# Optimization experiments

Measured on AMD Instinct MI355X. Metric: run time of the kernel, lower is better.

The kernel has to match this reference:

```python
import jax, jax.numpy as jnp
import numpy as np

BS, SEQ, IN, H, L = 32, 512, 1024, 1024, 2
STDV = 1.0 / np.sqrt(H)


def setup_inputs() -> dict:
    key = jax.random.key(0)
    ks = jax.random.split(key, 5)
    # params are uniform(-stdv, stdv) per reset_parameters
    u = lambda k, shape: jax.random.uniform(k, shape, jnp.float32, -STDV, STDV)
    return {
        "x": jax.random.normal(ks[0], (BS, SEQ, IN), jnp.float32),
        "w_ih": u(ks[1], (L, H, IN)),   # layer 0: [H, IN]; layer >0 uses [H, H] (IN==H here)
        "w_hh": u(ks[2], (L, H, H)),
        "b_ih": u(ks[3], (L, H)),
        "b_hh": u(ks[4], (L, H)),
    }


def _run_layer(x_sbH, w_ih_l, w_hh_l, b_ih_l, b_hh_l):
    # x_sbH: [seq, bs, in]. Precompute input projection as one GEMM.
    xproj = jnp.einsum('sbi,hi->sbh', x_sbH, w_ih_l) + b_ih_l + b_hh_l  # [seq, bs, H]

    def step(h, xp_t):
        # h_t = tanh(W_ih x_t + b_ih + W_hh h_{t-1} + b_hh)
        h_new = jnp.tanh(xp_t + h @ w_hh_l.T)
        return h_new, h_new

    h0 = jnp.zeros((x_sbH.shape[1], w_hh_l.shape[0]), x_sbH.dtype)
    h_last, hs = jax.lax.scan(step, h0, xproj)
    return hs, h_last  # hs: [seq, bs, H]


def reference(x, w_ih, w_hh, b_ih, b_hh):
    # batch_first: transpose to [seq, bs, in]
    h = jnp.transpose(x, (1, 0, 2))
    finals = []
    num_layers = w_ih.shape[0]
    for l in range(num_layers):
        h, h_last = _run_layer(h, w_ih[l], w_hh[l], b_ih[l], b_hh[l])
        finals.append(h_last)
    output = jnp.transpose(h, (1, 0, 2))           # [bs, seq, H]
    h_n = jnp.stack(finals, axis=0)                # [num_layers, bs, H]
    return output, h_n
```

## Files before the change

kernel.cpp:

```cpp
#include <hip/hip_runtime.h>

#define SEQL 512
#define BSZ  32
#define HID  1024
#define NWORK 48
#define NLAUNCH 384
#define HN_OFF 16777216

#define XPS_OFF 0u
#define H0B_OFF 33554432u
#define H1B_OFF 67108864u
#define FLG_OFF 100663296u
#define BOOT_OFF 100794368u

using f32x4  = __attribute__((ext_vector_type(4))) float;
using u16x8  = __attribute__((ext_vector_type(8))) unsigned short;
using u32x4  = __attribute__((ext_vector_type(4))) unsigned int;
using bf16x8 = __attribute__((ext_vector_type(8))) __bf16;

__device__ __forceinline__ f32x4 mfma16(u16x8 a, u16x8 b, f32x4 c) {
  return __builtin_amdgcn_mfma_f32_16x16x32_bf16(
      __builtin_bit_cast(bf16x8, a), __builtin_bit_cast(bf16x8, b), c, 0, 0, 0);
}

__device__ __forceinline__ unsigned short f2bf(float f) {
  unsigned u = __builtin_bit_cast(unsigned, f);
  u += 0x7fffu + ((u >> 16) & 1u);
  return (unsigned short)(u >> 16);
}
__device__ __forceinline__ unsigned short f2h(float f) {
  _Float16 h = (_Float16)f;
  return __builtin_bit_cast(unsigned short, h);
}
__device__ __forceinline__ float h2f(unsigned short u) {
  return (float)__builtin_bit_cast(_Float16, u);
}

__device__ __forceinline__ float tanh_fast(float x) {
  float cx = fminf(fmaxf(x, -15.f), 15.f);
  float e = __expf(2.f * cx);
  return __fdividef(e - 1.f, e + 1.f);
}

__device__ __forceinline__ void ld_tile_sc0(const unsigned short* base, u32x4 (&r)[16]) {
  const char* b0 = (const char*)base;
  const char* b1 = b0 + 16 * HID * 2;
  asm volatile(
    "global_load_dwordx4 %0, %16, off sc0\n\t"
    "global_load_dwordx4 %1, %16, off offset:64 sc0\n\t"
    "global_load_dwordx4 %2, %16, off offset:128 sc0\n\t"
    "global_load_dwordx4 %3, %16, off offset:192 sc0\n\t"
    "global_load_dwordx4 %4, %16, off offset:256 sc0\n\t"
    "global_load_dwordx4 %5, %16, off offset:320 sc0\n\t"
    "global_load_dwordx4 %6, %16, off offset:384 sc0\n\t"
    "global_load_dwordx4 %7, %16, off offset:448 sc0\n\t"
    "global_load_dwordx4 %8, %17, off sc0\n\t"
    "global_load_dwordx4 %9, %17, off offset:64 sc0\n\t"
    "global_load_dwordx4 %10, %17, off offset:128 sc0\n\t"
    "global_load_dwordx4 %11, %17, off offset:192 sc0\n\t"
    "global_load_dwordx4 %12, %17, off offset:256 sc0\n\t"
    "global_load_dwordx4 %13, %17, off offset:320 sc0\n\t"
    "global_load_dwordx4 %14, %17, off offset:384 sc0\n\t"
    "global_load_dwordx4 %15, %17, off offset:448 sc0\n\t"
    "s_waitcnt vmcnt(0)"
    : "=&v"(r[0]), "=&v"(r[1]), "=&v"(r[2]), "=&v"(r[3]),
      "=&v"(r[4]), "=&v"(r[5]), "=&v"(r[6]), "=&v"(r[7]),
      "=&v"(r[8]), "=&v"(r[9]), "=&v"(r[10]), "=&v"(r[11]),
      "=&v"(r[12]), "=&v"(r[13]), "=&v"(r[14]), "=&v"(r[15])
    : "v"(b0), "v"(b1)
    : "memory");
}

__device__ __forceinline__ u16x8 ld8h_sc0(const void* p) {
  u32x4 r;
  asm volatile("global_load_dwordx4 %0, %1, off sc0\n\ts_waitcnt vmcnt(0)"
               : "=&v"(r) : "v"(p) : "memory");
  return __builtin_bit_cast(u16x8, r);
}

__device__ __forceinline__ void flag_set(unsigned* p) {
  __hip_atomic_store(p, 1u, __ATOMIC_RELAXED, __HIP_MEMORY_SCOPE_AGENT);
}
__device__ __forceinline__ unsigned flag_get(const unsigned* p) {
  return __hip_atomic_load(p, __ATOMIC_RELAXED, __HIP_MEMORY_SCOPE_AGENT);
}
__device__ __forceinline__ void wave_wait4(const unsigned* flt, int wave, int lane) {
  const unsigned* p = flt + wave * 4 + (lane & 3);
  while (!__all(flag_get(p) != 0u)) {}
}
__device__ __forceinline__ void wave_wait1(const unsigned* p) {
  while (!__all(flag_get(p) != 0u)) {}
}

__global__ void init_kernel(unsigned* flg, int* boot) {
  int i = blockIdx.x * 256 + threadIdx.x;
  flg[i] = 0u;
  if (blockIdx.x == 0) {
    if (threadIdx.x < 16) boot[threadIdx.x] = 0;
    if (threadIdx.x == 16) boot[16] = -1;
  }
}

__global__ __launch_bounds__(256, 2)
void xproj_gemm(const float* __restrict__ X,
                const float* __restrict__ W,
                const float* __restrict__ bih,
                const float* __restrict__ bhh,
                unsigned short* __restrict__ out)
{
  __shared__ unsigned short sA[128 * 32];
  __shared__ unsigned short sB[128 * 32];
  const int tid  = threadIdx.x;
  const int lane = tid & 63;
  const int wave = tid >> 6;
  const int wm = wave >> 1, wn = wave & 1;
  const int bm = blockIdx.x >> 3;
  const int bn = blockIdx.x & 7;
  const int l15 = lane & 15;
  const int koff = (lane >> 4) * 8;
  const int srow = tid >> 2;
  const int skc  = (tid & 3) * 8;

  f32x4 acc[4][4];
#pragma unroll
  for (int i = 0; i < 4; ++i)
#pragma unroll
    for (int j = 0; j < 4; ++j) acc[i][j] = (f32x4)0.f;

  for (int k0 = 0; k0 < HID; k0 += 32) {
#pragma unroll
    for (int r = 0; r < 2; ++r) {
      int row = r * 64 + srow;
      int Mrow = bm * 128 + row;
      const float* src = X + ((size_t)(Mrow & 31) * SEQL + (Mrow >> 5)) * HID + k0 + skc;
      float4 a = ((const float4*)src)[0];
      float4 b = ((const float4*)src)[1];
      u16x8 av;
      av[0]=f2bf(a.x); av[1]=f2bf(a.y); av[2]=f2bf(a.z); av[3]=f2bf(a.w);
      av[4]=f2bf(b.x); av[5]=f2bf(b.y); av[6]=f2bf(b.z); av[7]=f2bf(b.w);
      *(u16x8*)&sA[row * 32 + skc] = av;

      const float* wsrc = W + (size_t)(bn * 128 + row) * HID + k0 + skc;
      float4 wa = ((const float4*)wsrc)[0];
      float4 wb = ((const float4*)wsrc)[1];
      u16x8 wv;
      wv[0]=f2bf(wa.x); wv[1]=f2bf(wa.y); wv[2]=f2bf(wa.z); wv[3]=f2bf(wa.w);
      wv[4]=f2bf(wb.x); wv[5]=f2bf(wb.y); wv[6]=f2bf(wb.z); wv[7]=f2bf(wb.w);
      *(u16x8*)&sB[row * 32 + skc] = wv;
    }
    __syncthreads();

    u16x8 af[4], bfr[4];
#pragma unroll
    for (int mt = 0; mt < 4; ++mt)
      af[mt] = *(const u16x8*)&sA[(wm * 64 + mt * 16 + l15) * 32 + koff];
#pragma unroll
    for (int nt = 0; nt < 4; ++nt)
      bfr[nt] = *(const u16x8*)&sB[(wn * 64 + nt * 16 + l15) * 32 + koff];
#pragma unroll
    for (int mt = 0; mt < 4; ++mt)
#pragma unroll
      for (int nt = 0; nt < 4; ++nt)
        acc[mt][nt] = mfma16(af[mt], bfr[nt], acc[mt][nt]);
    __syncthreads();
  }

#pragma unroll
  for (int nt = 0; nt < 4; ++nt) {
    int colg = bn * 128 + wn * 64 + nt * 16 + l15;
    float bias = bih[colg] + bhh[colg];
#pragma unroll
    for (int mt = 0; mt < 4; ++mt) {
#pragma unroll
      for (int i = 0; i < 4; ++i) {
        int rowg = bm * 128 + wm * 64 + mt * 16 + (lane >> 4) * 4 + i;
        out[(size_t)rowg * HID + colg] = f2h(acc[mt][nt][i] + bias);
      }
    }
  }
}

__global__ __launch_bounds__(256, 2)
void fused_scan(unsigned short* __restrict__ xps,
                const float* __restrict__ whh0,
                const float* __restrict__ wih1,
                const float* __restrict__ whh1,
                const float* __restrict__ bih1,
                const float* __restrict__ bhh1,
                unsigned short* __restrict__ h0b,
                unsigned short* __restrict__ h1b,
                float* __restrict__ out,
                unsigned* __restrict__ flg,
                int* __restrict__ boot)
{
  const int tid  = threadIdx.x;

  __shared__ int s_role;
  if (tid == 0) {
    unsigned xcc;
    asm volatile("s_getreg_b32 %0, hwreg(HW_REG_XCC_ID)" : "=s"(xcc));
    xcc &= 15u;
    int slot = __hip_atomic_fetch_add(&boot[(int)xcc], 1, __ATOMIC_RELAXED,
                                      __HIP_MEMORY_SCOPE_AGENT);
    if (slot == NWORK - 1) {
      int exp = -1;
      __hip_atomic_compare_exchange_strong(&boot[16], &exp, (int)xcc,
          __ATOMIC_RELAXED, __ATOMIC_RELAXED, __HIP_MEMORY_SCOPE_AGENT);
    }
    int ch;
    while ((ch = __hip_atomic_load(&boot[16], __ATOMIC_RELAXED,
                                   __HIP_MEMORY_SCOPE_AGENT)) < 0)
      __builtin_amdgcn_s_sleep(8);
    s_role = ((int)xcc == ch && slot < NWORK) ? slot : -1;
  }
  __syncthreads();
  const int role = s_role;
  if (role < 0) return;

  const int lane = tid & 63;
  const int wave = tid >> 6;
  const int l15  = lane & 15;
  const int l4   = lane >> 4;
  const int stage = role >> 4;
  const int wg    = role & 15;
  const int col0  = wg * 64;
  const int kbase = wave * 256;
  const int frow  = tid >> 3;
  const int fcb   = (tid & 7) * 8;
  const int laneoff = l15 * HID + kbase + l4 * 8;

  unsigned* flA = flg;
  unsigned* flB = flg + SEQL * 16;
  unsigned* flC = flg + 2 * SEQL * 16;

  __shared__ float red[4][32][68];

  const float* Wsl = (stage == 0) ? whh0 : (stage == 1) ? wih1 : whh1;
  u16x8 Bf[4][8];
#pragma unroll
  for (int nt = 0; nt < 4; ++nt)
#pragma unroll
    for (int ks = 0; ks < 8; ++ks) {
      const float* src = Wsl + (size_t)(col0 + nt * 16 + l15) * HID + kbase + ks * 32 + l4 * 8;
      float4 a = ((const float4*)src)[0];
      float4 b = ((const float4*)src)[1];
      u16x8 v;
      v[0]=f2bf(a.x); v[1]=f2bf(a.y); v[2]=f2bf(a.z); v[3]=f2bf(a.w);
      v[4]=f2bf(b.x); v[5]=f2bf(b.y); v[6]=f2bf(b.z); v[7]=f2bf(b.w);
      Bf[nt][ks] = v;
    }

  if (stage == 0) {
    u16x8 xh = *(const u16x8*)(xps + (size_t)frow * HID + col0 + fcb);
    for (int t = 0; t < SEQL; ++t) {
      f32x4 acc[2][4];
#pragma unroll
      for (int m = 0; m < 2; ++m)
#pragma unroll
        for (int n = 0; n < 4; ++n) acc[m][n] = (f32x4)0.f;
      if (t > 0) {
        wave_wait4(flA + (t - 1) * 16, wave, lane);
        u32x4 r[16];
        ld_tile_sc0(h0b + (size_t)(t - 1) * (BSZ * HID) + laneoff, r);
#pragma unroll
        for (int ks = 0; ks < 8; ++ks)
#pragma unroll
          for (int m = 0; m < 2; ++m)
#pragma unroll
            for (int n = 0; n < 4; ++n)
              acc[m][n] = mfma16(__builtin_bit_cast(u16x8, r[m * 8 + ks]), Bf[n][ks], acc[m][n]);
      }
#pragma unroll
      for (int m = 0; m < 2; ++m)
#pragma unroll
        for (int n = 0; n < 4; ++n)
#pragma unroll
          for (int q = 0; q < 4; ++q)
            red[wave][m * 16 + l4 * 4 + q][n * 16 + l15] = acc[m][n][q];
      __syncthreads();
      float hv[8];
#pragma unroll
      for (int jj = 0; jj < 2; ++jj) {
        float4 r0 = *(const float4*)&red[0][frow][fcb + jj * 4];
        float4 r1 = *(const float4*)&red[1][frow][fcb + jj * 4];
        float4 r2 = *(const float4*)&red[2][frow][fcb + jj * 4];
        float4 r3 = *(const float4*)&red[3][frow][fcb + jj * 4];
        hv[jj*4+0] = r0.x + r1.x + r2.x + r3.x;
        hv[jj*4+1] = r0.y + r1.y + r2.y + r3.y;
        hv[jj*4+2] = r0.z + r1.z + r2.z + r3.z;
        hv[jj*4+3] = r0.w + r1.w + r2.w + r3.w;
      }
#pragma unroll
      for (int j = 0; j < 8; ++j) hv[j] = tanh_fast(hv[j] + h2f((unsigned short)xh[j]));
      u16x8 hb;
#pragma unroll
      for (int j = 0; j < 8; ++j) hb[j] = f2bf(hv[j]);
      *(u16x8*)(h0b + (size_t)t * (BSZ * HID) + (size_t)frow * HID + col0 + fcb) = hb;
      if (t == SEQL - 1) {
        float* o = out + HN_OFF + (size_t)frow * HID + col0 + fcb;
        ((float4*)o)[0] = make_float4(hv[0], hv[1], hv[2], hv[3]);
        ((float4*)o)[1] = make_float4(hv[4], hv[5], hv[6], hv[7]);
      } else {
        xh = *(const u16x8*)(xps + ((size_t)(t + 1) * BSZ + frow) * HID + col0 + fcb);
      }
      asm volatile("s_waitcnt vmcnt(0)" ::: "memory");
      __syncthreads();
      if (tid == 0) flag_set(&flA[t * 16 + wg]);
    }
  } else if (stage == 1) {
    float bia[8];
#pragma unroll
    for (int j = 0; j < 8; ++j)
      bia[j] = bih1[col0 + fcb + j] + bhh1[col0 + fcb + j];
    for (int t = 0; t < SEQL; ++t) {
      wave_wait4(flA + t * 16, wave, lane);
      u32x4 r[16];
      ld_tile_sc0(h0b + (size_t)t * (BSZ * HID) + laneoff, r);
      f32x4 acc[2][4];
#pragma unroll
      for (int m = 0; m < 2; ++m)
#pragma unroll
        for (int n = 0; n < 4; ++n) acc[m][n] = (f32x4)0.f;
#pragma unroll
      for (int ks = 0; ks < 8; ++ks)
#pragma unroll
        for (int m = 0; m < 2; ++m)
#pragma unroll
          for (int n = 0; n < 4; ++n)
            acc[m][n] = mfma16(__builtin_bit_cast(u16x8, r[m * 8 + ks]), Bf[n][ks], acc[m][n]);
#pragma unroll
      for (int m = 0; m < 2; ++m)
#pragma unroll
        for (int n = 0; n < 4; ++n)
#pragma unroll
          for (int q = 0; q < 4; ++q)
            red[wave][m * 16 + l4 * 4 + q][n * 16 + l15] = acc[m][n][q];
      __syncthreads();
      float sv[8];
#pragma unroll
      for (int jj = 0; jj < 2; ++jj) {
        float4 r0 = *(const float4*)&red[0][frow][fcb + jj * 4];
        float4 r1 = *(const float4*)&red[1][frow][fcb + jj * 4];
        float4 r2 = *(const float4*)&red[2][frow][fcb + jj * 4];
        float4 r3 = *(const float4*)&red[3][frow][fcb + jj * 4];
        sv[jj*4+0] = r0.x + r1.x + r2.x + r3.x;
        sv[jj*4+1] = r0.y + r1.y + r2.y + r3.y;
        sv[jj*4+2] = r0.z + r1.z + r2.z + r3.z;
        sv[jj*4+3] = r0.w + r1.w + r2.w + r3.w;
      }
      u16x8 xo;
#pragma unroll
      for (int j = 0; j < 8; ++j) xo[j] = f2h(sv[j] + bia[j]);
      *(u16x8*)(xps + ((size_t)t * BSZ + frow) * HID + col0 + fcb) = xo;
      asm volatile("s_waitcnt vmcnt(0)" ::: "memory");
      __syncthreads();
      if (tid == 0) flag_set(&flB[t * 16 + wg]);
    }
  } else {
    for (int t = 0; t < SEQL; ++t) {
      f32x4 acc[2][4];
#pragma unroll
      for (int m = 0; m < 2; ++m)
#pragma unroll
        for (int n = 0; n < 4; ++n) acc[m][n] = (f32x4)0.f;
      if (t > 0) {
        wave_wait4(flC + (t - 1) * 16, wave, lane);
        u32x4 r[16];
        ld_tile_sc0(h1b + (size_t)(t - 1) * (BSZ * HID) + laneoff, r);
#pragma unroll
        for (int ks = 0; ks < 8; ++ks)
#pragma unroll
          for (int m = 0; m < 2; ++m)
#pragma unroll
            for (int n = 0; n < 4; ++n)
              acc[m][n] = mfma16(__builtin_bit_cast(u16x8, r[m * 8 + ks]), Bf[n][ks], acc[m][n]);
      }
#pragma unroll
      for (int m = 0; m < 2; ++m)
#pragma unroll
        for (int n = 0; n < 4; ++n)
#pragma unroll
          for (int q = 0; q < 4; ++q)
            red[wave][m * 16 + l4 * 4 + q][n * 16 + l15] = acc[m][n][q];
      __syncthreads();
      wave_wait1(&flB[t * 16 + wg]);
      u16x8 xq = ld8h_sc0(xps + ((size_t)t * BSZ + frow) * HID + col0 + fcb);
      float hv[8];
#pragma unroll
      for (int jj = 0; jj < 2; ++jj) {
        float4 r0 = *(const float4*)&red[0][frow][fcb + jj * 4];
        float4 r1 = *(const float4*)&red[1][frow][fcb + jj * 4];
        float4 r2 = *(const float4*)&red[2][frow][fcb + jj * 4];
        float4 r3 = *(const float4*)&red[3][frow][fcb + jj * 4];
        hv[jj*4+0] = r0.x + r1.x + r2.x + r3.x;
        hv[jj*4+1] = r0.y + r1.y + r2.y + r3.y;
        hv[jj*4+2] = r0.z + r1.z + r2.z + r3.z;
        hv[jj*4+3] = r0.w + r1.w + r2.w + r3.w;
      }
#pragma unroll
      for (int j = 0; j < 8; ++j) hv[j] = tanh_fast(hv[j] + h2f((unsigned short)xq[j]));
      u16x8 hb;
#pragma unroll
      for (int j = 0; j < 8; ++j) hb[j] = f2bf(hv[j]);
      *(u16x8*)(h1b + (size_t)t * (BSZ * HID) + (size_t)frow * HID + col0 + fcb) = hb;
      float* op = out + ((size_t)frow * SEQL + t) * HID + col0 + fcb;
      ((float4*)op)[0] = make_float4(hv[0], hv[1], hv[2], hv[3]);
      ((float4*)op)[1] = make_float4(hv[4], hv[5], hv[6], hv[7]);
      if (t == SEQL - 1) {
        float* o = out + HN_OFF + BSZ * HID + (size_t)frow * HID + col0 + fcb;
        ((float4*)o)[0] = make_float4(hv[0], hv[1], hv[2], hv[3]);
        ((float4*)o)[1] = make_float4(hv[4], hv[5], hv[6], hv[7]);
      }
      asm volatile("s_waitcnt vmcnt(0)" ::: "memory");
      __syncthreads();
      if (tid == 0) flag_set(&flC[t * 16 + wg]);
    }
  }
}

extern "C" void kernel_launch(void* const* d_in, const int* in_sizes, int n_in,
                              void* d_out, int out_size, void* d_ws, size_t ws_size,
                              hipStream_t stream) {
  const float* x    = (const float*)d_in[0];
  const float* w_ih = (const float*)d_in[1];
  const float* w_hh = (const float*)d_in[2];
  const float* b_ih = (const float*)d_in[3];
  const float* b_hh = (const float*)d_in[4];
  float* out = (float*)d_out;
  char* ws = (char*)d_ws;

  unsigned short* xps = (unsigned short*)(ws + XPS_OFF);
  unsigned short* h0b = (unsigned short*)(ws + H0B_OFF);
  unsigned short* h1b = (unsigned short*)(ws + H1B_OFF);
  unsigned* flg       = (unsigned*)(ws + FLG_OFF);
  int* boot           = (int*)(ws + BOOT_OFF);

  init_kernel<<<96, 256, 0, stream>>>(flg, boot);
  xproj_gemm<<<1024, 256, 0, stream>>>(x, w_ih, b_ih, b_hh, xps);
  fused_scan<<<NLAUNCH, 256, 0, stream>>>(xps, w_hh,
      w_ih + (size_t)HID * HID, w_hh + (size_t)HID * HID,
      b_ih + HID, b_hh + HID, h0b, h1b, out, flg, boot);
}
```

Before: 3.788 ms.

## Replace flag handshakes with sentinel-polled data and merge layer-1 stages

Drops the per-timestep flag arrays. Consumers now poll the hidden-state buffers themselves, which are prefilled with a 0xAA sentinel pattern, and accept a tile once no 32-bit word still matches the sentinel. Producers write with agent-scope atomic 8-byte stores and no longer wait on vmcnt or set a flag. The layer-1 input projection and recurrence stages are merged into one workgroup that holds both weight slices in registers, so 32 workgroups run instead of 48 and the intermediate xps round-trip is gone. The costs are a 64 MB memset on every call, more register pressure (launch bounds lowered to 1), and a small risk of a false wait if a real bf16 pair happens to equal the sentinel.

```diff
diff --git a/kernel.cpp b/kernel.cpp
--- a/kernel.cpp
+++ b/kernel.cpp
@@ -3,19 +3,21 @@
 #define SEQL 512
 #define BSZ  32
 #define HID  1024
-#define NWORK 48
+#define NWORK 32
 #define NLAUNCH 384
 #define HN_OFF 16777216
 
 #define XPS_OFF 0u
 #define H0B_OFF 33554432u
 #define H1B_OFF 67108864u
-#define FLG_OFF 100663296u
-#define BOOT_OFF 100794368u
+#define BOOT_OFF 100663296u
+
+#define SENT32 0xAAAAAAAAu
 
 using f32x4  = __attribute__((ext_vector_type(4))) float;
 using u16x8  = __attribute__((ext_vector_type(8))) unsigned short;
 using u32x4  = __attribute__((ext_vector_type(4))) unsigned int;
+using u64x2  = __attribute__((ext_vector_type(2))) unsigned long long;
 using bf16x8 = __attribute__((ext_vector_type(8))) __bf16;
 
 __device__ __forceinline__ f32x4 mfma16(u16x8 a, u16x8 b, f32x4 c) {
@@ -42,63 +44,45 @@
   return __fdividef(e - 1.f, e + 1.f);
 }
 
-__device__ __forceinline__ void ld_tile_sc0(const unsigned short* base, u32x4 (&r)[16]) {
-  const char* b0 = (const char*)base;
-  const char* b1 = b0 + 16 * HID * 2;
-  asm volatile(
-    "global_load_dwordx4 %0, %16, off sc0\n\t"
-    "global_load_dwordx4 %1, %16, off offset:64 sc0\n\t"
-    "global_load_dwordx4 %2, %16, off offset:128 sc0\n\t"
-    "global_load_dwordx4 %3, %16, off offset:192 sc0\n\t"
-    "global_load_dwordx4 %4, %16, off offset:256 sc0\n\t"
-    "global_load_dwordx4 %5, %16, off offset:320 sc0\n\t"
-    "global_load_dwordx4 %6, %16, off offset:384 sc0\n\t"
-    "global_load_dwordx4 %7, %16, off offset:448 sc0\n\t"
-    "global_load_dwordx4 %8, %17, off sc0\n\t"
-    "global_load_dwordx4 %9, %17, off offset:64 sc0\n\t"
-    "global_load_dwordx4 %10, %17, off offset:128 sc0\n\t"
-    "global_load_dwordx4 %11, %17, off offset:192 sc0\n\t"
-    "global_load_dwordx4 %12, %17, off offset:256 sc0\n\t"
-    "global_load_dwordx4 %13, %17, off offset:320 sc0\n\t"
-    "global_load_dwordx4 %14, %17, off offset:384 sc0\n\t"
-    "global_load_dwordx4 %15, %17, off offset:448 sc0\n\t"
-    "s_waitcnt vmcnt(0)"
-    : "=&v"(r[0]), "=&v"(r[1]), "=&v"(r[2]), "=&v"(r[3]),
-      "=&v"(r[4]), "=&v"(r[5]), "=&v"(r[6]), "=&v"(r[7]),
-      "=&v"(r[8]), "=&v"(r[9]), "=&v"(r[10]), "=&v"(r[11]),
-      "=&v"(r[12]), "=&v"(r[13]), "=&v"(r[14]), "=&v"(r[15])
-    : "v"(b0), "v"(b1)
-    : "memory");
-}
-
-__device__ __forceinline__ u16x8 ld8h_sc0(const void* p) {
-  u32x4 r;
-  asm volatile("global_load_dwordx4 %0, %1, off sc0\n\ts_waitcnt vmcnt(0)"
-               : "=&v"(r) : "v"(p) : "memory");
-  return __builtin_bit_cast(u16x8, r);
-}
-
-__device__ __forceinline__ void flag_set(unsigned* p) {
-  __hip_atomic_store(p, 1u, __ATOMIC_RELAXED, __HIP_MEMORY_SCOPE_AGENT);
-}
-__device__ __forceinline__ unsigned flag_get(const unsigned* p) {
+__device__ __forceinline__ unsigned long long ld8_agent(const unsigned long long* p) {
   return __hip_atomic_load(p, __ATOMIC_RELAXED, __HIP_MEMORY_SCOPE_AGENT);
 }
-__device__ __forceinline__ void wave_wait4(const unsigned* flt, int wave, int lane) {
-  const unsigned* p = flt + wave * 4 + (lane & 3);
-  while (!__all(flag_get(p) != 0u)) {}
-}
-__device__ __forceinline__ void wave_wait1(const unsigned* p) {
-  while (!__all(flag_get(p) != 0u)) {}
-}
-
-__global__ void init_kernel(unsigned* flg, int* boot) {
-  int i = blockIdx.x * 256 + threadIdx.x;
-  flg[i] = 0u;
-  if (blockIdx.x == 0) {
-    if (threadIdx.x < 16) boot[threadIdx.x] = 0;
-    if (threadIdx.x == 16) boot[16] = -1;
+__device__ __forceinline__ void st8_agent(unsigned long long* p, unsigned long long v) {
+  __hip_atomic_store(p, v, __ATOMIC_RELAXED, __HIP_MEMORY_SCOPE_AGENT);
+}
+__device__ __forceinline__ void st_frag(unsigned short* dst, u16x8 hb) {
+  u64x2 q = __builtin_bit_cast(u64x2, hb);
+  st8_agent((unsigned long long*)dst, q[0]);
+  st8_agent((unsigned long long*)dst + 1, q[1]);
+}
+
+__device__ __forceinline__ void tile_poll8(const unsigned short* rowbase, u16x8 (&Af)[8]) {
+  const unsigned long long* b8 = (const unsigned long long*)rowbase;
+  for (;;) {
+    unsigned long long v[16];
+#pragma unroll
+    for (int ks = 0; ks < 8; ++ks) {
+      v[2 * ks]     = ld8_agent(b8 + ks * 8);
+      v[2 * ks + 1] = ld8_agent(b8 + ks * 8 + 1);
+    }
+    int good = 1;
+#pragma unroll
+    for (int c = 0; c < 16; ++c)
+      good &= ((unsigned)v[c] != SENT32) & ((unsigned)(v[c] >> 32) != SENT32);
+    if (__all(good)) {
+#pragma unroll
+      for (int ks = 0; ks < 8; ++ks) {
+        u64x2 q; q[0] = v[2 * ks]; q[1] = v[2 * ks + 1];
+        Af[ks] = __builtin_bit_cast(u16x8, q);
+      }
+      return;
+    }
+    __builtin_amdgcn_s_sleep(1);
   }
+}
+
+__global__ void init_kernel(int* boot) {
+  if (threadIdx.x < 17) boot[threadIdx.x] = (threadIdx.x == 16) ? -1 : 0;
 }
 
 __global__ __launch_bounds__(256, 2)
@@ -180,8 +164,8 @@
   }
 }
 
-__global__ __launch_bounds__(256, 2)
-void fused_scan(unsigned short* __restrict__ xps,
+__global__ __launch_bounds__(256, 1)
+void fused_scan(const unsigned short* __restrict__ xps,
                 const float* __restrict__ whh0,
                 const float* __restrict__ wih1,
                 const float* __restrict__ whh1,
@@ -190,7 +174,6 @@
                 unsigned short* __restrict__ h0b,
                 unsigned short* __restrict__ h1b,
                 float* __restrict__ out,
-                unsigned* __restrict__ flg,
                 int* __restrict__ boot)
 {
   const int tid  = threadIdx.x;
@@ -221,7 +204,6 @@
   const int wave = tid >> 6;
   const int l15  = lane & 15;
   const int l4   = lane >> 4;
-  const int stage = role >> 4;
   const int wg    = role & 15;
   const int col0  = wg * 64;
   const int kbase = wave * 256;
@@ -229,29 +211,25 @@
   const int fcb   = (tid & 7) * 8;
   const int laneoff = l15 * HID + kbase + l4 * 8;
 
-  unsigned* flA = flg;
-  unsigned* flB = flg + SEQL * 16;
-  unsigned* flC = flg + 2 * SEQL * 16;
-
   __shared__ float red[4][32][68];
 
-  const float* Wsl = (stage == 0) ? whh0 : (stage == 1) ? wih1 : whh1;
-  u16x8 Bf[4][8];
-#pragma unroll
-  for (int nt = 0; nt < 4; ++nt)
-#pragma unroll
-    for (int ks = 0; ks < 8; ++ks) {
-      const float* src = Wsl + (size_t)(col0 + nt * 16 + l15) * HID + kbase + ks * 32 + l4 * 8;
-      float4 a = ((const float4*)src)[0];
-      float4 b = ((const float4*)src)[1];
-      u16x8 v;
-      v[0]=f2bf(a.x); v[1]=f2bf(a.y); v[2]=f2bf(a.z); v[3]=f2bf(a.w);
-      v[4]=f2bf(b.x); v[5]=f2bf(b.y); v[6]=f2bf(b.z); v[7]=f2bf(b.w);
-      Bf[nt][ks] = v;
-    }
-
-  if (stage == 0) {
+  if (role < 16) {
+    u16x8 Bf[4][8];
+#pragma unroll
+    for (int nt = 0; nt < 4; ++nt)
+#pragma unroll
+      for (int ks = 0; ks < 8; ++ks) {
+        const float* src = whh0 + (size_t)(col0 + nt * 16 + l15) * HID + kbase + ks * 32 + l4 * 8;
+        float4 a = ((const float4*)src)[0];
+        float4 b = ((const float4*)src)[1];
+        u16x8 v;
+        v[0]=f2bf(a.x); v[1]=f2bf(a.y); v[2]=f2bf(a.z); v[3]=f2bf(a.w);
+        v[4]=f2bf(b.x); v[5]=f2bf(b.y); v[6]=f2bf(b.z); v[7]=f2bf(b.w);
+        Bf[nt][ks] = v;
+      }
+
     u16x8 xh = *(const u16x8*)(xps + (size_t)frow * HID + col0 + fcb);
+
     for (int t = 0; t < SEQL; ++t) {
       f32x4 acc[2][4];
 #pragma unroll
@@ -259,16 +237,17 @@
 #pragma unroll
         for (int n = 0; n < 4; ++n) acc[m][n] = (f32x4)0.f;
       if (t > 0) {
-        wave_wait4(flA + (t - 1) * 16, wave, lane);
-        u32x4 r[16];
-        ld_tile_sc0(h0b + (size_t)(t - 1) * (BSZ * HID) + laneoff, r);
-#pragma unroll
-        for (int ks = 0; ks < 8; ++ks)
-#pragma unroll
-          for (int m = 0; m < 2; ++m)
+        const unsigned short* hp = h0b + (size_t)(t - 1) * (BSZ * HID) + laneoff;
+#pragma unroll
+        for (int m = 0; m < 2; ++m) {
+          u16x8 Af[8];
+          tile_poll8(hp + m * 16 * HID, Af);
+#pragma unroll
+          for (int ks = 0; ks < 8; ++ks)
 #pragma unroll
             for (int n = 0; n < 4; ++n)
-              acc[m][n] = mfma16(__builtin_bit_cast(u16x8, r[m * 8 + ks]), Bf[n][ks], acc[m][n]);
+              acc[m][n] = mfma16(Af[ks], Bf[n][ks], acc[m][n]);
+        }
       }
 #pragma unroll
       for (int m = 0; m < 2; ++m)
@@ -295,7 +274,7 @@
       u16x8 hb;
 #pragma unroll
       for (int j = 0; j < 8; ++j) hb[j] = f2bf(hv[j]);
-      *(u16x8*)(h0b + (size_t)t * (BSZ * HID) + (size_t)frow * HID + col0 + fcb) = hb;
+      st_frag(h0b + (size_t)t * (BSZ * HID) + (size_t)frow * HID + col0 + fcb, hb);
       if (t == SEQL - 1) {
         float* o = out + HN_OFF + (size_t)frow * HID + col0 + fcb;
         ((float4*)o)[0] = make_float4(hv[0], hv[1], hv[2], hv[3]);
@@ -303,31 +282,66 @@
       } else {
         xh = *(const u16x8*)(xps + ((size_t)(t + 1) * BSZ + frow) * HID + col0 + fcb);
       }
-      asm volatile("s_waitcnt vmcnt(0)" ::: "memory");
       __syncthreads();
-      if (tid == 0) flag_set(&flA[t * 16 + wg]);
-    }
-  } else if (stage == 1) {
+    }
+  } else {
+    u16x8 Bih[4][8], Bhh[4][8];
+#pragma unroll
+    for (int nt = 0; nt < 4; ++nt)
+#pragma unroll
+      for (int ks = 0; ks < 8; ++ks) {
+        const float* s1 = wih1 + (size_t)(col0 + nt * 16 + l15) * HID + kbase + ks * 32 + l4 * 8;
+        float4 a = ((const float4*)s1)[0];
+        float4 b = ((const float4*)s1)[1];
+        u16x8 v;
+        v[0]=f2bf(a.x); v[1]=f2bf(a.y); v[2]=f2bf(a.z); v[3]=f2bf(a.w);
+        v[4]=f2bf(b.x); v[5]=f2bf(b.y); v[6]=f2bf(b.z); v[7]=f2bf(b.w);
+        Bih[nt][ks] = v;
+        const float* s2 = whh1 + (size_t)(col0 + nt * 16 + l15) * HID + kbase + ks * 32 + l4 * 8;
+        float4 c = ((const float4*)s2)[0];
+        float4 d = ((const float4*)s2)[1];
+        u16x8 w;
+        w[0]=f2bf(c.x); w[1]=f2bf(c.y); w[2]=f2bf(c.z); w[3]=f2bf(c.w);
+        w[4]=f2bf(d.x); w[5]=f2bf(d.y); w[6]=f2bf(d.z); w[7]=f2bf(d.w);
+        Bhh[nt][ks] = w;
+      }
     float bia[8];
 #pragma unroll
     for (int j = 0; j < 8; ++j)
       bia[j] = bih1[col0 + fcb + j] + bhh1[col0 + fcb + j];
+
     for (int t = 0; t < SEQL; ++t) {
-      wave_wait4(flA + t * 16, wave, lane);
-      u32x4 r[16];
-      ld_tile_sc0(h0b + (size_t)t * (BSZ * HID) + laneoff, r);
       f32x4 acc[2][4];
 #pragma unroll
       for (int m = 0; m < 2; ++m)
 #pragma unroll
         for (int n = 0; n < 4; ++n) acc[m][n] = (f32x4)0.f;
-#pragma unroll
-      for (int ks = 0; ks < 8; ++ks)
-#pragma unroll
-        for (int m = 0; m < 2; ++m)
-#pragma unroll
-          for (int n = 0; n < 4; ++n)
-            acc[m][n] = mfma16(__builtin_bit_cast(u16x8, r[m * 8 + ks]), Bf[n][ks], acc[m][n]);
+      {
+        const unsigned short* hp = h0b + (size_t)t * (BSZ * HID) + laneoff;
+#pragma unroll
+        for (int m = 0; m < 2; ++m) {
+          u16x8 Af[8];
+          tile_poll8(hp + m * 16 * HID, Af);
+#pragma unroll
+          for (int ks = 0; ks < 8; ++ks)
+#pragma unroll
+            for (int n = 0; n < 4; ++n)
+              acc[m][n] = mfma16(Af[ks], Bih[n][ks], acc[m][n]);
+        }
+      }
+      if (t > 0) {
+        const unsigned short* hp = h1b + (size_t)(t - 1) * (BSZ * HID) + laneoff;
+#pragma unroll
+        for (int m = 0; m < 2; ++m) {
+          u16x8 Af[8];
+          tile_poll8(hp + m * 16 * HID, Af);
+#pragma unroll
+          for (int ks = 0; ks < 8; ++ks)
+#pragma unroll
+            for (int n = 0; n < 4; ++n)
+              acc[m][n] = mfma16(Af[ks], Bhh[n][ks], acc[m][n]);
+        }
+      }
 #pragma unroll
       for (int m = 0; m < 2; ++m)
 #pragma unroll
@@ -336,55 +350,6 @@
           for (int q = 0; q < 4; ++q)
             red[wave][m * 16 + l4 * 4 + q][n * 16 + l15] = acc[m][n][q];
       __syncthreads();
-      float sv[8];
-#pragma unroll
-      for (int jj = 0; jj < 2; ++jj) {
-        float4 r0 = *(const float4*)&red[0][frow][fcb + jj * 4];
-        float4 r1 = *(const float4*)&red[1][frow][fcb + jj * 4];
-        float4 r2 = *(const float4*)&red[2][frow][fcb + jj * 4];
-        float4 r3 = *(const float4*)&red[3][frow][fcb + jj * 4];
-        sv[jj*4+0] = r0.x + r1.x + r2.x + r3.x;
-        sv[jj*4+1] = r0.y + r1.y + r2.y + r3.y;
-        sv[jj*4+2] = r0.z + r1.z + r2.z + r3.z;
-        sv[jj*4+3] = r0.w + r1.w + r2.w + r3.w;
-      }
-      u16x8 xo;
-#pragma unroll
-      for (int j = 0; j < 8; ++j) xo[j] = f2h(sv[j] + bia[j]);
-      *(u16x8*)(xps + ((size_t)t * BSZ + frow) * HID + col0 + fcb) = xo;
-      asm volatile("s_waitcnt vmcnt(0)" ::: "memory");
-      __syncthreads();
-      if (tid == 0) flag_set(&flB[t * 16 + wg]);
-    }
-  } else {
-    for (int t = 0; t < SEQL; ++t) {
-      f32x4 acc[2][4];
-#pragma unroll
-      for (int m = 0; m < 2; ++m)
-#pragma unroll
-        for (int n = 0; n < 4; ++n) acc[m][n] = (f32x4)0.f;
-      if (t > 0) {
-        wave_wait4(flC + (t - 1) * 16, wave, lane);
-        u32x4 r[16];
-        ld_tile_sc0(h1b + (size_t)(t - 1) * (BSZ * HID) + laneoff, r);
-#pragma unroll
-        for (int ks = 0; ks < 8; ++ks)
-#pragma unroll
-          for (int m = 0; m < 2; ++m)
-#pragma unroll
-            for (int n = 0; n < 4; ++n)
-              acc[m][n] = mfma16(__builtin_bit_cast(u16x8, r[m * 8 + ks]), Bf[n][ks], acc[m][n]);
-      }
-#pragma unroll
-      for (int m = 0; m < 2; ++m)
-#pragma unroll
-        for (int n = 0; n < 4; ++n)
-#pragma unroll
-          for (int q = 0; q < 4; ++q)
-            red[wave][m * 16 + l4 * 4 + q][n * 16 + l15] = acc[m][n][q];
-      __syncthreads();
-      wave_wait1(&flB[t * 16 + wg]);
-      u16x8 xq = ld8h_sc0(xps + ((size_t)t * BSZ + frow) * HID + col0 + fcb);
       float hv[8];
 #pragma unroll
       for (int jj = 0; jj < 2; ++jj) {
@@ -398,11 +363,11 @@
         hv[jj*4+3] = r0.w + r1.w + r2.w + r3.w;
       }
 #pragma unroll
-      for (int j = 0; j < 8; ++j) hv[j] = tanh_fast(hv[j] + h2f((unsigned short)xq[j]));
+      for (int j = 0; j < 8; ++j) hv[j] = tanh_fast(hv[j] + bia[j]);
       u16x8 hb;
 #pragma unroll
       for (int j = 0; j < 8; ++j) hb[j] = f2bf(hv[j]);
-      *(u16x8*)(h1b + (size_t)t * (BSZ * HID) + (size_t)frow * HID + col0 + fcb) = hb;
+      st_frag(h1b + (size_t)t * (BSZ * HID) + (size_t)frow * HID + col0 + fcb, hb);
       float* op = out + ((size_t)frow * SEQL + t) * HID + col0 + fcb;
       ((float4*)op)[0] = make_float4(hv[0], hv[1], hv[2], hv[3]);
       ((float4*)op)[1] = make_float4(hv[4], hv[5], hv[6], hv[7]);
@@ -411,9 +376,7 @@
         ((float4*)o)[0] = make_float4(hv[0], hv[1], hv[2], hv[3]);
         ((float4*)o)[1] = make_float4(hv[4], hv[5], hv[6], hv[7]);
       }
-      asm volatile("s_waitcnt vmcnt(0)" ::: "memory");
       __syncthreads();
-      if (tid == 0) flag_set(&flC[t * 16 + wg]);
     }
   }
 }
@@ -432,12 +395,13 @@
   unsigned short* xps = (unsigned short*)(ws + XPS_OFF);
   unsigned short* h0b = (unsigned short*)(ws + H0B_OFF);
   unsigned short* h1b = (unsigned short*)(ws + H1B_OFF);
-  unsigned* flg       = (unsigned*)(ws + FLG_OFF);
   int* boot           = (int*)(ws + BOOT_OFF);
 
-  init_kernel<<<96, 256, 0, stream>>>(flg, boot);
+  hipMemsetAsync(ws + H0B_OFF, 0xAA, 67108864u, stream);
+
+  init_kernel<<<1, 64, 0, stream>>>(boot);
   xproj_gemm<<<1024, 256, 0, stream>>>(x, w_ih, b_ih, b_hh, xps);
   fused_scan<<<NLAUNCH, 256, 0, stream>>>(xps, w_hh,
       w_ih + (size_t)HID * HID, w_hh + (size_t)HID * HID,
-      b_ih + HID, b_hh + HID, h0b, h1b, out, flg, boot);
-}
+      b_ih + HID, b_hh + HID, h0b, h1b, out, boot);
+}
```

Result: slower. 4.703 ms (+24.2%).
